# Kernel optimization log

Measured on AMD Instinct MI355X. Metric: run time of the kernel, lower is better.

## Reference

```python
import jax, jax.numpy as jnp
import numpy as np

NBATCH, NA = 16, 1024


def setup_inputs() -> dict:
    key = jax.random.key(0)
    # Batched dense operator parameters; the linear module applies the
    # symmetrized matrix M = 0.5*(A + A^T) (Hermitian operator -> real spectrum).
    A = jax.random.normal(key, (NBATCH, NA, NA), dtype=jnp.float32)
    return {"A": A, "nlowest": 16}


def reference(A, nlowest):
    # EigenModule.forward with method='exacteig': full symmetric
    # eigendecomposition, then keep the `nlowest` lowest eigenpairs.
    M = 0.5 * (A + jnp.swapaxes(A, -1, -2))  # (B, na, na) symmetric
    eigvals, eigvecs = jnp.linalg.eigh(M)    # ascending eigenvalues
    return eigvals[:, :nlowest], eigvecs[:, :, :nlowest]
```

## Files before the change

### kernel.cpp

```cpp
#include <hip/hip_runtime.h>
#include <stdint.h>
#include <math.h>

#define NN 1024
#define NB 16
#define NLOW 16
#define PNB 32
#define JCH 128
#define GMID 4

__device__ inline void patchvals(float alphaf, double rest, float& albe, float& beta, float& taut) {
    if (rest == 0.0) { albe = 0.f; beta = alphaf; taut = 0.f; return; }
    double a = (double)alphaf;
    double nrm = sqrt(a * a + rest);
    double b = (a >= 0.0) ? -nrm : nrm;
    double ab = a - b;
    albe = (float)ab;
    beta = (float)b;
    taut = (float)(-1.0 / (b * ab));
}

__global__ void k_symmetrize(const float* A, float* M) {
    int64_t t = (int64_t)blockIdx.x * blockDim.x + threadIdx.x;
    if (t >= (int64_t)NB * NN * NN) return;
    int b = (int)(t / (NN * NN));
    int rc = (int)(t % (NN * NN));
    int r = rc / NN, c = rc % NN;
    if (r > c) return;
    const float* Ab = A + (int64_t)b * NN * NN;
    float s = 0.5f * (Ab[(int64_t)r * NN + c] + Ab[(int64_t)c * NN + r]);
    float* Mb = M + (int64_t)b * NN * NN;
    Mb[(int64_t)r * NN + c] = s;
    Mb[(int64_t)c * NN + r] = s;
}

__global__ void k_zeroinit(float* wv, double* norm2A, double* dotwA) {
    int t = blockIdx.x * 256 + threadIdx.x;
    if (t < NB * NN) { wv[t] = 0.f; norm2A[t] = 0.0; dotwA[t] = 0.0; }
}

__global__ __launch_bounds__(256) void k_midA(const float* Vp, float* Wp, float* wv,
                                              const float* tauA, double* dotwA,
                                              const double* c1A, const double* c2A,
                                              int k0, int j) {
    int b = blockIdx.x, y = blockIdx.y, tid = threadIdx.x;
    int jp = j - 1, kp = k0 + jp, m0 = NN - 1 - k0;
    __shared__ float g1[PNB], g2[PNB];
    __shared__ double redd[256];
    if (tid < jp) {
        double kap = 0.5 * (double)tauA[b * NN + k0 + tid] * dotwA[b * NN + k0 + tid];
        double c2 = c2A[b * PNB + tid];
        g1[tid] = (float)(c1A[b * PNB + tid] - 2.0 * kap * c2);
        g2[tid] = (float)c2;
    }
    __syncthreads();
    float taut = tauA[b * NN + kp];
    const float* ujp = Vp + ((int64_t)b * PNB + jp) * NN;
    float* wcol = Wp + ((int64_t)b * PNB + jp) * NN;
    double dacc = 0.0;
    for (int i = jp + y * 256 + tid; i < m0; i += GMID * 256) {
        float wr = wv[b * NN + i];
        wv[b * NN + i] = 0.f;
        for (int t = 0; t < jp; ++t)
            wr -= Vp[((int64_t)b * PNB + t) * NN + i] * g1[t]
                + Wp[((int64_t)b * PNB + t) * NN + i] * g2[t];
        float wf = taut * wr;
        wcol[i] = wf;
        dacc += (double)wf * (double)ujp[i];
    }
    redd[tid] = dacc; __syncthreads();
    for (int s = 128; s > 0; s >>= 1) {
        if (tid < s) redd[tid] += redd[tid + s];
        __syncthreads();
    }
    if (tid == 0) atomicAdd(&dotwA[b * NN + kp], redd[0]);
}

__global__ __launch_bounds__(256) void k_midB(float* M, float* Vp, const float* Wp,
                                              float* dA, const float* tauA, const double* dotwA,
                                              double* norm2A, float* alphaA,
                                              int k0, int j) {
    int b = blockIdx.x, y = blockIdx.y, tid = threadIdx.x;
    int k = k0 + j, m0 = NN - 1 - k0;
    float* Mb = M + (int64_t)b * NN * NN;
    __shared__ float h1[PNB], h2[PNB], h3[PNB];
    __shared__ double redd[256];
    if (tid < j) {
        int r = j - 1;
        float ur = Vp[((int64_t)b * PNB + tid) * NN + r];
        float wr = Wp[((int64_t)b * PNB + tid) * NN + r];
        float kap = (float)(0.5 * (double)tauA[b * NN + k0 + tid] * dotwA[b * NN + k0 + tid]);
        float wbar = wr - kap * ur;
        h1[tid] = wbar - kap * ur;
        h2[tid] = ur;
        h3[tid] = ur * wbar;
    }
    __syncthreads();
    if (y == 0 && tid == 0) {
        float dk = Mb[(int64_t)k * NN + k];
        for (int t = 0; t < j; ++t) dk -= 2.f * h3[t];
        dA[b * NN + k] = dk;
    }
    double nacc = 0.0;
    float* ucol = Vp + ((int64_t)b * PNB + j) * NN;
    for (int i = j + y * 256 + tid; i < m0; i += GMID * 256) {
        float x = Mb[(int64_t)(k0 + 1 + i) * NN + k];
        for (int t = 0; t < j; ++t)
            x -= Vp[((int64_t)b * PNB + t) * NN + i] * h1[t]
               + Wp[((int64_t)b * PNB + t) * NN + i] * h2[t];
        ucol[i] = x;
        Mb[(int64_t)(k0 + 1 + i) * NN + k] = x;
        if (i == j) alphaA[b * NN + k] = x;
        else nacc += (double)x * (double)x;
    }
    redd[tid] = nacc; __syncthreads();
    for (int s = 128; s > 0; s >>= 1) {
        if (tid < s) redd[tid] += redd[tid + s];
        __syncthreads();
    }
    if (tid == 0) atomicAdd(&norm2A[b * NN + k], redd[0]);
}

__global__ __launch_bounds__(256) void k_symv(float* M, float* Vp, const float* Wp,
                                              float* wv, float* tauA, float* eA,
                                              const float* alphaA, const double* norm2A,
                                              double* c1A, double* c2A,
                                              int k0, int j, int nr, int nc) {
    int b = blockIdx.x, y = blockIdx.y, tid = threadIdx.x;
    int k = k0 + j, m = NN - 1 - k, base = k + 1, m0 = NN - 1 - k0;
    float albe, beta, taut;
    patchvals(alphaA[b * NN + k], norm2A[b * NN + k], albe, beta, taut);
    float* Mb = M + (int64_t)b * NN * NN;
    float* ucol = Vp + ((int64_t)b * PNB + j) * NN;
    __shared__ float vs[JCH];
    __shared__ double r1[256], r2[256];
    if (y < nr * nc) {
        if (y == 0 && tid == 0) {
            ucol[j] = albe;
            Mb[(int64_t)(k0 + 1 + j) * NN + k] = albe;
            eA[b * NN + k] = beta;
            tauA[b * NN + k] = taut;
        }
        int ir = y % nr, ic = y / nr;
        int i = ir * 256 + tid;
        int jg0 = ic * JCH, jg1 = min(m, jg0 + JCH);
        for (int t = tid; t < jg1 - jg0; t += 256) vs[t] = ucol[jg0 + t + j];
        __syncthreads();
        if (tid == 0 && jg0 == 0) vs[0] = albe;
        __syncthreads();
        if (i < m) {
            const float* p = Mb + (int64_t)(base + jg0) * NN + base + i;
            float acc = 0.f;
            for (int jg = jg0; jg < jg1; ++jg, p += NN) acc += (*p) * vs[jg - jg0];
            atomicAdd(&wv[b * NN + i + j], acc);
        }
    } else {
        int t = y - nr * nc;
        const float* ut = Vp + ((int64_t)b * PNB + t) * NN;
        const float* wt = Wp + ((int64_t)b * PNB + t) * NN;
        double a1 = 0.0, a2 = 0.0;
        for (int i = j + tid; i < m0; i += 256) {
            float uj = (i == j) ? albe : ucol[i];
            a1 += (double)wt[i] * (double)uj;
            a2 += (double)ut[i] * (double)uj;
        }
        r1[tid] = a1; r2[tid] = a2; __syncthreads();
        for (int s = 128; s > 0; s >>= 1) {
            if (tid < s) { r1[tid] += r1[tid + s]; r2[tid] += r2[tid + s]; }
            __syncthreads();
        }
        if (tid == 0) { c1A[b * PNB + t] = r1[0]; c2A[b * PNB + t] = r2[0]; }
    }
}

__global__ __launch_bounds__(256) void k_update(float* M, const float* Vp, const float* Wp,
                                                const float* tauA, const double* dotwA,
                                                int k0, int nbe) {
    int b = blockIdx.x;
    int s = k0 + nbe, m2 = NN - s;
    int r0 = blockIdx.y * 64, c0 = blockIdx.z * 64;
    if (r0 >= m2 || c0 >= m2) return;
    __shared__ float Vr[PNB][64], Wr[PNB][64], Vc[PNB][64], Wc[PNB][64];
    __shared__ float kap[PNB];
    int tid = threadIdx.x;
    if (tid < nbe)
        kap[tid] = (float)(0.5 * (double)tauA[b * NN + k0 + tid] * dotwA[b * NN + k0 + tid]);
    __syncthreads();
    int rowoff = nbe - 1;
    for (int idx = tid; idx < nbe * 64; idx += 256) {
        int t = idx >> 6, x = idx & 63;
        const float* vp = Vp + ((int64_t)b * PNB + t) * NN;
        const float* wp = Wp + ((int64_t)b * PNB + t) * NN;
        int rr = r0 + x, cc = c0 + x;
        float vr = (rr < m2) ? vp[rowoff + rr] : 0.f;
        float wr = (rr < m2) ? wp[rowoff + rr] : 0.f;
        float vc = (cc < m2) ? vp[rowoff + cc] : 0.f;
        float wc = (cc < m2) ? wp[rowoff + cc] : 0.f;
        Vr[t][x] = vr; Wr[t][x] = wr - kap[t] * vr;
        Vc[t][x] = vc; Wc[t][x] = wc - kap[t] * vc;
    }
    __syncthreads();
    int tx = tid & 15, ty = tid >> 4;
    float accv[4][4] = {};
    for (int t = 0; t < nbe; ++t) {
        float va[4], wa[4], vb4[4], wb4[4];
#pragma unroll
        for (int a = 0; a < 4; ++a) {
            va[a] = Vr[t][ty * 4 + a]; wa[a] = Wr[t][ty * 4 + a];
            vb4[a] = Vc[t][tx * 4 + a]; wb4[a] = Wc[t][tx * 4 + a];
        }
#pragma unroll
        for (int a = 0; a < 4; ++a)
#pragma unroll
            for (int c = 0; c < 4; ++c) accv[a][c] += va[a] * wb4[c] + wa[a] * vb4[c];
    }
    float* Mb = M + (int64_t)b * NN * NN;
    for (int a = 0; a < 4; ++a) {
        int r = r0 + ty * 4 + a;
        if (r >= m2) break;
        for (int c = 0; c < 4; ++c) {
            int cc = c0 + tx * 4 + c;
            if (cc >= m2) continue;
            Mb[(int64_t)(s + r) * NN + (s + cc)] -= accv[a][c];
        }
    }
}

__global__ void k_extract2(const float* M, float* dA, float* eA) {
    int b = blockIdx.x;
    if (threadIdx.x == 0) {
        const float* Mb = M + (int64_t)b * NN * NN;
        dA[b * NN + NN - 2] = Mb[(int64_t)(NN - 2) * NN + NN - 2];
        dA[b * NN + NN - 1] = Mb[(int64_t)(NN - 1) * NN + NN - 1];
        eA[b * NN + NN - 2] = Mb[(int64_t)(NN - 1) * NN + NN - 2];
    }
}

__global__ void k_bisect(const float* dA, const float* eA, double* lam, float* out) {
    int p = threadIdx.x;
    int b = p >> 4, j = p & 15;
    const float* d = dA + b * NN;
    const float* e = eA + b * NN;
    double lo = 1e30, hi = -1e30;
    for (int i = 0; i < NN; ++i) {
        double di = (double)d[i];
        double r = 0.0;
        if (i > 0) r += fabs((double)e[i - 1]);
        if (i < NN - 1) r += fabs((double)e[i]);
        lo = fmin(lo, di - r);
        hi = fmax(hi, di + r);
    }
    lo -= 1e-3; hi += 1e-3;
    for (int it = 0; it < 50; ++it) {
        double x = 0.5 * (lo + hi);
        int cnt = 0;
        double q = (double)d[0] - x;
        if (q < 0.0) cnt++;
        for (int i = 1; i < NN; ++i) {
            double ei = (double)e[i - 1];
            double den = q;
            if (fabs(den) < 1e-30) den = (den < 0.0) ? -1e-30 : 1e-30;
            q = ((double)d[i] - x) - ei * ei / den;
            if (q < 0.0) cnt++;
        }
        if (cnt >= j + 1) hi = x; else lo = x;
    }
    double l = 0.5 * (lo + hi);
    lam[p] = l;
    out[b * NLOW + j] = (float)l;
}

__global__ void k_invit(const float* dA, const float* eA, const double* lam,
                        float* vtri, double* U0, double* U1, double* U2,
                        double* LM, float* PV, double* XV) {
    int p = blockIdx.x * blockDim.x + threadIdx.x;
    if (p >= NB * NLOW) return;
    int b = p / NLOW;
    const float* d = dA + b * NN;
    const float* e = eA + b * NN;
    double lambda = lam[p];
    double* dd  = U0 + (int64_t)p * NN;
    double* du  = U1 + (int64_t)p * NN;
    double* du2 = U2 + (int64_t)p * NN;
    double* dl  = LM + (int64_t)p * NN;
    float*  pv  = PV + (int64_t)p * NN;
    double* X   = XV + (int64_t)p * NN;

    for (int i = 0; i < NN; ++i) dd[i] = (double)d[i] - lambda;
    for (int i = 0; i < NN - 1; ++i) { du[i] = (double)e[i]; dl[i] = (double)e[i]; }
    du[NN - 1] = 0.0; dl[NN - 1] = 0.0;

    for (int i = 0; i < NN - 1; ++i) {
        if (fabs(dd[i]) >= fabs(dl[i])) {
            pv[i] = 0.f;
            double fact = (dd[i] != 0.0) ? dl[i] / dd[i] : 0.0;
            dl[i] = fact;
            dd[i + 1] -= fact * du[i];
            du2[i] = 0.0;
        } else {
            pv[i] = 1.f;
            double fact = dd[i] / dl[i];
            dd[i] = dl[i];
            dl[i] = fact;
            double temp = du[i];
            du[i] = dd[i + 1];
            dd[i + 1] = temp - fact * dd[i + 1];
            if (i < NN - 2) { du2[i] = du[i + 1]; du[i + 1] = -fact * du[i + 1]; }
            else du2[i] = 0.0;
        }
    }
    for (int i = 0; i < NN; ++i)
        if (fabs(dd[i]) < 1e-300) dd[i] = (dd[i] < 0.0) ? -1e-300 : 1e-300;

    for (int i = 0; i < NN; ++i) {
        uint32_t h = ((uint32_t)i * 2654435761u) ^ ((uint32_t)p * 40503u);
        h = h * 1664525u + 1013904223u;
        X[i] = 1.0 + 1e-3 * ((double)(h & 2047) / 1024.0 - 1.0);
    }
    for (int iter = 0; iter < 2; ++iter) {
        for (int i = 0; i < NN - 1; ++i) {
            if (pv[i] == 0.f) X[i + 1] -= dl[i] * X[i];
            else { double t = X[i]; X[i] = X[i + 1]; X[i + 1] = t - dl[i] * X[i]; }
        }
        X[NN - 1] /= dd[NN - 1];
        X[NN - 2] = (X[NN - 2] - du[NN - 2] * X[NN - 1]) / dd[NN - 2];
        for (int i = NN - 3; i >= 0; --i)
            X[i] = (X[i] - du[i] * X[i + 1] - du2[i] * X[i + 2]) / dd[i];
        double nrm = 0.0;
        for (int i = 0; i < NN; ++i) nrm += X[i] * X[i];
        double inv = 1.0 / sqrt(fmax(nrm, 1e-300));
        for (int i = 0; i < NN; ++i) X[i] *= inv;
    }
    float* vt = vtri + (int64_t)p * NN;
    for (int i = 0; i < NN; ++i) vt[i] = (float)X[i];
}

__global__ void k_gs(float* vtri) {
    int b = blockIdx.x;
    float* V = vtri + (int64_t)b * NLOW * NN;
    __shared__ double red[256];
    for (int j = 0; j < NLOW; ++j) {
        float* vj = V + j * NN;
        for (int i2 = 0; i2 < j; ++i2) {
            const float* vi = V + i2 * NN;
            double acc = 0.0;
            for (int t = threadIdx.x; t < NN; t += 256) acc += (double)vi[t] * (double)vj[t];
            red[threadIdx.x] = acc; __syncthreads();
            for (int s = 128; s > 0; s >>= 1) {
                if ((int)threadIdx.x < s) red[threadIdx.x] += red[threadIdx.x + s];
                __syncthreads();
            }
            float r = (float)red[0];
            for (int t = threadIdx.x; t < NN; t += 256) vj[t] -= r * vi[t];
            __syncthreads();
        }
        double acc = 0.0;
        for (int t = threadIdx.x; t < NN; t += 256) acc += (double)vj[t] * (double)vj[t];
        red[threadIdx.x] = acc; __syncthreads();
        for (int s = 128; s > 0; s >>= 1) {
            if ((int)threadIdx.x < s) red[threadIdx.x] += red[threadIdx.x + s];
            __syncthreads();
        }
        float inv = (float)(1.0 / sqrt(fmax(red[0], 1e-300)));
        for (int t = threadIdx.x; t < NN; t += 256) vj[t] *= inv;
        __syncthreads();
    }
}

__global__ __launch_bounds__(512) void k_backtransform(const float* M, const float* tauA,
                                                       const float* vtri, float* out) {
    int b = blockIdx.x;
    int pass = blockIdx.y;
    int w = threadIdx.x >> 6;
    int lane = threadIdx.x & 63;
    int j = pass * 8 + w;
    __shared__ float xs[8][NN];
    __shared__ float us[NN];
    const float* Mb = M + (int64_t)b * NN * NN;
    for (int i = lane; i < NN; i += 64)
        xs[w][i] = vtri[((int64_t)b * NLOW + j) * NN + i];
    __syncthreads();
    for (int k = NN - 3; k >= 0; --k) {
        int m = NN - 1 - k;
        for (int t = threadIdx.x; t < (unsigned)m; t += 512)
            us[t] = Mb[(int64_t)(k + 1 + t) * NN + k];
        __syncthreads();
        float tauk = tauA[b * NN + k];
        float acc = 0.f;
        for (int t = lane; t < m; t += 64) acc += us[t] * xs[w][k + 1 + t];
        for (int off = 32; off > 0; off >>= 1) acc += __shfl_xor(acc, off);
        float s = tauk * acc;
        for (int t = lane; t < m; t += 64) xs[w][k + 1 + t] -= s * us[t];
        __syncthreads();
    }
    float mx = -1.f; int mi = 0;
    for (int i = lane; i < NN; i += 64) {
        float a = fabsf(xs[w][i]);
        if (a > mx) { mx = a; mi = i; }
    }
    for (int off = 32; off > 0; off >>= 1) {
        float omx = __shfl_xor(mx, off);
        int omi = __shfl_xor(mi, off);
        if (omx > mx || (omx == mx && omi < mi)) { mx = omx; mi = omi; }
    }
    float sgn = (xs[w][mi] < 0.f) ? -1.f : 1.f;
    for (int i = lane; i < NN; i += 64)
        out[256 + ((int64_t)(b * NN + i)) * NLOW + j] = sgn * xs[w][i];
}

extern "C" void kernel_launch(void* const* d_in, const int* in_sizes, int n_in,
                              void* d_out, int out_size, void* d_ws, size_t ws_size,
                              hipStream_t stream) {
    const float* A = (const float*)d_in[0];
    float* out = (float*)d_out;

    char* base = (char*)d_ws;
    size_t off = 0;
    auto alloc = [&](size_t bytes) -> void* {
        void* p = (void*)(base + off);
        off = (off + bytes + 255) & ~(size_t)255;
        return p;
    };
    double* lam  = (double*)alloc(sizeof(double) * NB * NLOW);
    double* u0   = (double*)alloc(sizeof(double) * (size_t)NB * NLOW * NN);
    double* u1   = (double*)alloc(sizeof(double) * (size_t)NB * NLOW * NN);
    double* u2   = (double*)alloc(sizeof(double) * (size_t)NB * NLOW * NN);
    double* lmul = (double*)alloc(sizeof(double) * (size_t)NB * NLOW * NN);
    double* xv   = (double*)alloc(sizeof(double) * (size_t)NB * NLOW * NN);
    float* pivf  = (float*)alloc(sizeof(float) * (size_t)NB * NLOW * NN);
    float* vtri  = (float*)alloc(sizeof(float) * (size_t)NB * NLOW * NN);
    float* tau   = (float*)alloc(sizeof(float) * NB * NN);
    float* evec  = (float*)alloc(sizeof(float) * NB * NN);
    float* dvec  = (float*)alloc(sizeof(float) * NB * NN);
    float* wv    = (float*)alloc(sizeof(float) * NB * NN);
    float* alphaA = (float*)alloc(sizeof(float) * NB * NN);
    double* norm2A = (double*)alloc(sizeof(double) * NB * NN);
    double* dotwA  = (double*)alloc(sizeof(double) * NB * NN);
    double* c1A    = (double*)alloc(sizeof(double) * NB * PNB);
    double* c2A    = (double*)alloc(sizeof(double) * NB * PNB);
    float* Vp    = (float*)alloc(sizeof(float) * (size_t)NB * PNB * NN);
    float* Wp    = (float*)alloc(sizeof(float) * (size_t)NB * PNB * NN);
    size_t small_end = off;

    float* M;
    if (ws_size >= small_end + sizeof(float) * (size_t)NB * NN * NN)
        M = (float*)alloc(sizeof(float) * (size_t)NB * NN * NN);
    else
        M = (float*)d_in[0];

    int grid_sym = (NB * NN * NN) / 256;
    k_symmetrize<<<grid_sym, 256, 0, stream>>>(A, M);
    k_zeroinit<<<(NB * NN + 255) / 256, 256, 0, stream>>>(wv, norm2A, dotwA);

    for (int k0 = 0; k0 < NN - 2; k0 += PNB) {
        int jmax = NN - 2 - k0; if (jmax > PNB) jmax = PNB;
        for (int j = 0; j < jmax; ++j) {
            if (j > 0)
                k_midA<<<dim3(NB, GMID), 256, 0, stream>>>(Vp, Wp, wv, tau, dotwA, c1A, c2A, k0, j);
            k_midB<<<dim3(NB, GMID), 256, 0, stream>>>(M, Vp, Wp, dvec, tau, dotwA, norm2A, alphaA, k0, j);
            int k = k0 + j, m = NN - 1 - k;
            int nr = (m + 255) / 256, nc = (m + JCH - 1) / JCH;
            k_symv<<<dim3(NB, nr * nc + j), 256, 0, stream>>>(M, Vp, Wp, wv, tau, evec,
                                                              alphaA, norm2A, c1A, c2A,
                                                              k0, j, nr, nc);
        }
        k_midA<<<dim3(NB, GMID), 256, 0, stream>>>(Vp, Wp, wv, tau, dotwA, c1A, c2A, k0, jmax);
        int s = k0 + jmax, m2 = NN - s;
        if (m2 > 0) {
            dim3 gu(NB, (unsigned)((m2 + 63) / 64), (unsigned)((m2 + 63) / 64));
            k_update<<<gu, 256, 0, stream>>>(M, Vp, Wp, tau, dotwA, k0, jmax);
        }
    }

    k_extract2<<<NB, 64, 0, stream>>>(M, dvec, evec);
    k_bisect<<<1, 256, 0, stream>>>(dvec, evec, lam, out);
    k_invit<<<4, 64, 0, stream>>>(dvec, evec, lam, vtri, u0, u1, u2, lmul, pivf, xv);
    k_gs<<<NB, 256, 0, stream>>>(vtri);
    dim3 gI(NB, 2);
    k_backtransform<<<gI, 512, 0, stream>>>(M, tau, vtri, out);
}
```

Measured before the change: 41.04 ms.

## Fuse panel mid-step kernels into one per-batch block and store Householder vectors contiguously

Merges k_midA and k_midB into a single 1024-thread kernel per batch. It computes the Householder reflector in-block, which removes the norm/alpha atomics and the patchvals recomputation, and moves the c1/c2 dot products out of the symv launch into that kernel. k_symv becomes a pure matvec with a larger column chunk. A contiguous copy of each Householder vector (Urev) is also stored when workspace permits, so back-transformation reads rows instead of strided columns. This cuts launch count and per-step synchronization at the cost of fewer, larger blocks in the mid step and an extra matrix-sized workspace buffer.

```diff
diff --git a/kernel.cpp b/kernel.cpp
--- a/kernel.cpp
+++ b/kernel.cpp
@@ -6,19 +6,7 @@
 #define NB 16
 #define NLOW 16
 #define PNB 32
-#define JCH 128
-#define GMID 4
-
-__device__ inline void patchvals(float alphaf, double rest, float& albe, float& beta, float& taut) {
-    if (rest == 0.0) { albe = 0.f; beta = alphaf; taut = 0.f; return; }
-    double a = (double)alphaf;
-    double nrm = sqrt(a * a + rest);
-    double b = (a >= 0.0) ? -nrm : nrm;
-    double ab = a - b;
-    albe = (float)ab;
-    beta = (float)b;
-    taut = (float)(-1.0 / (b * ab));
-}
+#define JCH 256
 
 __global__ void k_symmetrize(const float* A, float* M) {
     int64_t t = (int64_t)blockIdx.x * blockDim.x + threadIdx.x;
@@ -34,57 +22,63 @@
     Mb[(int64_t)c * NN + r] = s;
 }
 
-__global__ void k_zeroinit(float* wv, double* norm2A, double* dotwA) {
+__global__ void k_zeroinit(float* wv) {
     int t = blockIdx.x * 256 + threadIdx.x;
-    if (t < NB * NN) { wv[t] = 0.f; norm2A[t] = 0.0; dotwA[t] = 0.0; }
-}
-
-__global__ __launch_bounds__(256) void k_midA(const float* Vp, float* Wp, float* wv,
-                                              const float* tauA, double* dotwA,
-                                              const double* c1A, const double* c2A,
-                                              int k0, int j) {
-    int b = blockIdx.x, y = blockIdx.y, tid = threadIdx.x;
-    int jp = j - 1, kp = k0 + jp, m0 = NN - 1 - k0;
-    __shared__ float g1[PNB], g2[PNB];
-    __shared__ double redd[256];
-    if (tid < jp) {
-        double kap = 0.5 * (double)tauA[b * NN + k0 + tid] * dotwA[b * NN + k0 + tid];
-        double c2 = c2A[b * PNB + tid];
-        g1[tid] = (float)(c1A[b * PNB + tid] - 2.0 * kap * c2);
-        g2[tid] = (float)c2;
-    }
-    __syncthreads();
-    float taut = tauA[b * NN + kp];
-    const float* ujp = Vp + ((int64_t)b * PNB + jp) * NN;
-    float* wcol = Wp + ((int64_t)b * PNB + jp) * NN;
-    double dacc = 0.0;
-    for (int i = jp + y * 256 + tid; i < m0; i += GMID * 256) {
-        float wr = wv[b * NN + i];
-        wv[b * NN + i] = 0.f;
-        for (int t = 0; t < jp; ++t)
-            wr -= Vp[((int64_t)b * PNB + t) * NN + i] * g1[t]
-                + Wp[((int64_t)b * PNB + t) * NN + i] * g2[t];
-        float wf = taut * wr;
-        wcol[i] = wf;
-        dacc += (double)wf * (double)ujp[i];
-    }
-    redd[tid] = dacc; __syncthreads();
-    for (int s = 128; s > 0; s >>= 1) {
-        if (tid < s) redd[tid] += redd[tid + s];
-        __syncthreads();
-    }
-    if (tid == 0) atomicAdd(&dotwA[b * NN + kp], redd[0]);
-}
-
-__global__ __launch_bounds__(256) void k_midB(float* M, float* Vp, const float* Wp,
-                                              float* dA, const float* tauA, const double* dotwA,
-                                              double* norm2A, float* alphaA,
-                                              int k0, int j) {
-    int b = blockIdx.x, y = blockIdx.y, tid = threadIdx.x;
-    int k = k0 + j, m0 = NN - 1 - k0;
+    if (t < NB * NN) wv[t] = 0.f;
+}
+
+__global__ __launch_bounds__(1024) void k_mid(float* M, float* Vp, float* Wp, float* wv,
+                                              float* tauA, float* eA, float* dA,
+                                              double* dotwA, double* c1A, double* c2A,
+                                              float* Urev, int useU,
+                                              int k0, int j, int do_col) {
+    int b = blockIdx.x, tid = threadIdx.x;
+    int wid = tid >> 6, lane = tid & 63;
+    int m0 = NN - 1 - k0;
     float* Mb = M + (int64_t)b * NN * NN;
-    __shared__ float h1[PNB], h2[PNB], h3[PNB];
-    __shared__ double redd[256];
+    __shared__ double sred[16];
+    __shared__ float g1[PNB], g2[PNB], h1[PNB], h2[PNB], h3[PNB];
+    __shared__ float shu[NN];
+    __shared__ float sc_alpha, sc_albe;
+
+    if (j > 0) {
+        int jp = j - 1, kp = k0 + jp;
+        if (tid < jp) {
+            double kap = 0.5 * (double)tauA[b * NN + k0 + tid] * dotwA[b * NN + k0 + tid];
+            double c2 = c2A[b * PNB + tid];
+            g1[tid] = (float)(c1A[b * PNB + tid] - 2.0 * kap * c2);
+            g2[tid] = (float)c2;
+        }
+        __syncthreads();
+        float taut = tauA[b * NN + kp];
+        const float* ujp = Vp + ((int64_t)b * PNB + jp) * NN;
+        float* wcol = Wp + ((int64_t)b * PNB + jp) * NN;
+        int i = jp + tid;
+        double dacc = 0.0;
+        if (i < m0) {
+            float wr = wv[b * NN + i];
+            wv[b * NN + i] = 0.f;
+            for (int t = 0; t < jp; ++t)
+                wr -= Vp[((int64_t)b * PNB + t) * NN + i] * g1[t]
+                    + Wp[((int64_t)b * PNB + t) * NN + i] * g2[t];
+            float wf = taut * wr;
+            wcol[i] = wf;
+            dacc = (double)wf * (double)ujp[i];
+        }
+        for (int o = 32; o; o >>= 1) dacc += __shfl_xor(dacc, o);
+        if (lane == 0) sred[wid] = dacc;
+        __syncthreads();
+        if (tid == 0) {
+            double tot = 0.0;
+            for (int w = 0; w < 16; ++w) tot += sred[w];
+            dotwA[b * NN + kp] = tot;
+        }
+        __syncthreads();
+    }
+
+    if (!do_col) return;
+
+    int k = k0 + j;
     if (tid < j) {
         int r = j - 1;
         float ur = Vp[((int64_t)b * PNB + tid) * NN + r];
@@ -96,81 +90,80 @@
         h3[tid] = ur * wbar;
     }
     __syncthreads();
-    if (y == 0 && tid == 0) {
+    int i = j + tid;
+    float x = 0.f;
+    if (i < m0) {
+        x = Mb[(int64_t)(k0 + 1 + i) * NN + k];
+        for (int t = 0; t < j; ++t)
+            x -= Vp[((int64_t)b * PNB + t) * NN + i] * h1[t]
+               + Wp[((int64_t)b * PNB + t) * NN + i] * h2[t];
+    }
+    if (tid == 0) sc_alpha = x;
+    double nacc = (i > j && i < m0) ? (double)x * (double)x : 0.0;
+    for (int o = 32; o; o >>= 1) nacc += __shfl_xor(nacc, o);
+    if (lane == 0) sred[wid] = nacc;
+    __syncthreads();
+    if (tid == 0) {
+        double rest = 0.0;
+        for (int w = 0; w < 16; ++w) rest += sred[w];
+        float albe, beta, taut;
+        if (rest == 0.0) { albe = 0.f; beta = sc_alpha; taut = 0.f; }
+        else {
+            double a = (double)sc_alpha;
+            double nrm = sqrt(a * a + rest);
+            double bt = (a >= 0.0) ? -nrm : nrm;
+            double ab = a - bt;
+            albe = (float)ab;
+            beta = (float)bt;
+            taut = (float)(-1.0 / (bt * ab));
+        }
         float dk = Mb[(int64_t)k * NN + k];
         for (int t = 0; t < j; ++t) dk -= 2.f * h3[t];
         dA[b * NN + k] = dk;
-    }
-    double nacc = 0.0;
-    float* ucol = Vp + ((int64_t)b * PNB + j) * NN;
-    for (int i = j + y * 256 + tid; i < m0; i += GMID * 256) {
-        float x = Mb[(int64_t)(k0 + 1 + i) * NN + k];
-        for (int t = 0; t < j; ++t)
-            x -= Vp[((int64_t)b * PNB + t) * NN + i] * h1[t]
-               + Wp[((int64_t)b * PNB + t) * NN + i] * h2[t];
-        ucol[i] = x;
-        Mb[(int64_t)(k0 + 1 + i) * NN + k] = x;
-        if (i == j) alphaA[b * NN + k] = x;
-        else nacc += (double)x * (double)x;
-    }
-    redd[tid] = nacc; __syncthreads();
-    for (int s = 128; s > 0; s >>= 1) {
-        if (tid < s) redd[tid] += redd[tid + s];
-        __syncthreads();
-    }
-    if (tid == 0) atomicAdd(&norm2A[b * NN + k], redd[0]);
-}
-
-__global__ __launch_bounds__(256) void k_symv(float* M, float* Vp, const float* Wp,
-                                              float* wv, float* tauA, float* eA,
-                                              const float* alphaA, const double* norm2A,
-                                              double* c1A, double* c2A,
-                                              int k0, int j, int nr, int nc) {
-    int b = blockIdx.x, y = blockIdx.y, tid = threadIdx.x;
-    int k = k0 + j, m = NN - 1 - k, base = k + 1, m0 = NN - 1 - k0;
-    float albe, beta, taut;
-    patchvals(alphaA[b * NN + k], norm2A[b * NN + k], albe, beta, taut);
-    float* Mb = M + (int64_t)b * NN * NN;
-    float* ucol = Vp + ((int64_t)b * PNB + j) * NN;
-    __shared__ float vs[JCH];
-    __shared__ double r1[256], r2[256];
-    if (y < nr * nc) {
-        if (y == 0 && tid == 0) {
-            ucol[j] = albe;
-            Mb[(int64_t)(k0 + 1 + j) * NN + k] = albe;
-            eA[b * NN + k] = beta;
-            tauA[b * NN + k] = taut;
-        }
-        int ir = y % nr, ic = y / nr;
-        int i = ir * 256 + tid;
-        int jg0 = ic * JCH, jg1 = min(m, jg0 + JCH);
-        for (int t = tid; t < jg1 - jg0; t += 256) vs[t] = ucol[jg0 + t + j];
-        __syncthreads();
-        if (tid == 0 && jg0 == 0) vs[0] = albe;
-        __syncthreads();
-        if (i < m) {
-            const float* p = Mb + (int64_t)(base + jg0) * NN + base + i;
-            float acc = 0.f;
-            for (int jg = jg0; jg < jg1; ++jg, p += NN) acc += (*p) * vs[jg - jg0];
-            atomicAdd(&wv[b * NN + i + j], acc);
-        }
-    } else {
-        int t = y - nr * nc;
+        tauA[b * NN + k] = taut;
+        eA[b * NN + k] = beta;
+        sc_albe = albe;
+    }
+    __syncthreads();
+    if (i < m0) {
+        float val = (tid == 0) ? sc_albe : x;
+        Vp[((int64_t)b * PNB + j) * NN + i] = val;
+        Mb[(int64_t)(k0 + 1 + i) * NN + k] = val;
+        if (useU) Urev[((int64_t)b * NN + k) * NN + (i - j)] = val;
+        shu[i] = val;
+    }
+    __syncthreads();
+    for (int t = wid; t < j; t += 16) {
         const float* ut = Vp + ((int64_t)b * PNB + t) * NN;
         const float* wt = Wp + ((int64_t)b * PNB + t) * NN;
         double a1 = 0.0, a2 = 0.0;
-        for (int i = j + tid; i < m0; i += 256) {
-            float uj = (i == j) ? albe : ucol[i];
-            a1 += (double)wt[i] * (double)uj;
-            a2 += (double)ut[i] * (double)uj;
-        }
-        r1[tid] = a1; r2[tid] = a2; __syncthreads();
-        for (int s = 128; s > 0; s >>= 1) {
-            if (tid < s) { r1[tid] += r1[tid + s]; r2[tid] += r2[tid + s]; }
-            __syncthreads();
-        }
-        if (tid == 0) { c1A[b * PNB + t] = r1[0]; c2A[b * PNB + t] = r2[0]; }
-    }
+        for (int i2 = j + lane; i2 < m0; i2 += 64) {
+            float uj = shu[i2];
+            a1 += (double)wt[i2] * (double)uj;
+            a2 += (double)ut[i2] * (double)uj;
+        }
+        for (int o = 32; o; o >>= 1) { a1 += __shfl_xor(a1, o); a2 += __shfl_xor(a2, o); }
+        if (lane == 0) { c1A[b * PNB + t] = a1; c2A[b * PNB + t] = a2; }
+    }
+}
+
+__global__ __launch_bounds__(256) void k_symv(const float* M, const float* Vp, float* wv,
+                                              int k0, int j) {
+    int b = blockIdx.x;
+    int k = k0 + j, m = NN - 1 - k, base = k + 1;
+    int i = blockIdx.y * 256 + threadIdx.x;
+    int jg0 = blockIdx.z * JCH;
+    int jg1 = min(m, jg0 + JCH);
+    __shared__ float vs[JCH];
+    const float* vcol = Vp + ((int64_t)b * PNB + j) * NN;
+    for (int t = threadIdx.x; t < jg1 - jg0; t += 256) vs[t] = vcol[jg0 + t + j];
+    __syncthreads();
+    if (i >= m) return;
+    const float* Mb = M + (int64_t)b * NN * NN;
+    const float* p = Mb + (int64_t)(base + jg0) * NN + base + i;
+    float acc = 0.f;
+    for (int jg = jg0; jg < jg1; ++jg, p += NN) acc += (*p) * vs[jg - jg0];
+    atomicAdd(&wv[b * NN + i + j], acc);
 }
 
 __global__ __launch_bounds__(256) void k_update(float* M, const float* Vp, const float* Wp,
@@ -367,7 +360,8 @@
     }
 }
 
-__global__ __launch_bounds__(512) void k_backtransform(const float* M, const float* tauA,
+__global__ __launch_bounds__(512) void k_backtransform(const float* M, const float* Urev,
+                                                       int useU, const float* tauA,
                                                        const float* vtri, float* out) {
     int b = blockIdx.x;
     int pass = blockIdx.y;
@@ -382,8 +376,13 @@
     __syncthreads();
     for (int k = NN - 3; k >= 0; --k) {
         int m = NN - 1 - k;
-        for (int t = threadIdx.x; t < (unsigned)m; t += 512)
-            us[t] = Mb[(int64_t)(k + 1 + t) * NN + k];
+        if (useU) {
+            const float* ur = Urev + ((int64_t)b * NN + k) * NN;
+            for (int t = threadIdx.x; t < (unsigned)m; t += 512) us[t] = ur[t];
+        } else {
+            for (int t = threadIdx.x; t < (unsigned)m; t += 512)
+                us[t] = Mb[(int64_t)(k + 1 + t) * NN + k];
+        }
         __syncthreads();
         float tauk = tauA[b * NN + k];
         float acc = 0.f;
@@ -433,38 +432,42 @@
     float* evec  = (float*)alloc(sizeof(float) * NB * NN);
     float* dvec  = (float*)alloc(sizeof(float) * NB * NN);
     float* wv    = (float*)alloc(sizeof(float) * NB * NN);
-    float* alphaA = (float*)alloc(sizeof(float) * NB * NN);
-    double* norm2A = (double*)alloc(sizeof(double) * NB * NN);
-    double* dotwA  = (double*)alloc(sizeof(double) * NB * NN);
-    double* c1A    = (double*)alloc(sizeof(double) * NB * PNB);
-    double* c2A    = (double*)alloc(sizeof(double) * NB * PNB);
+    double* dotwA = (double*)alloc(sizeof(double) * NB * NN);
+    double* c1A   = (double*)alloc(sizeof(double) * NB * PNB);
+    double* c2A   = (double*)alloc(sizeof(double) * NB * PNB);
     float* Vp    = (float*)alloc(sizeof(float) * (size_t)NB * PNB * NN);
     float* Wp    = (float*)alloc(sizeof(float) * (size_t)NB * PNB * NN);
     size_t small_end = off;
+    size_t mat_bytes = sizeof(float) * (size_t)NB * NN * NN;
 
     float* M;
-    if (ws_size >= small_end + sizeof(float) * (size_t)NB * NN * NN)
-        M = (float*)alloc(sizeof(float) * (size_t)NB * NN * NN);
+    if (ws_size >= small_end + mat_bytes)
+        M = (float*)alloc(mat_bytes);
     else
         M = (float*)d_in[0];
 
+    float* Urev = nullptr;
+    int useU = 0;
+    if (ws_size >= off + mat_bytes) {
+        Urev = (float*)alloc(mat_bytes);
+        useU = 1;
+    }
+
     int grid_sym = (NB * NN * NN) / 256;
     k_symmetrize<<<grid_sym, 256, 0, stream>>>(A, M);
-    k_zeroinit<<<(NB * NN + 255) / 256, 256, 0, stream>>>(wv, norm2A, dotwA);
+    k_zeroinit<<<(NB * NN + 255) / 256, 256, 0, stream>>>(wv);
 
     for (int k0 = 0; k0 < NN - 2; k0 += PNB) {
         int jmax = NN - 2 - k0; if (jmax > PNB) jmax = PNB;
         for (int j = 0; j < jmax; ++j) {
-            if (j > 0)
-                k_midA<<<dim3(NB, GMID), 256, 0, stream>>>(Vp, Wp, wv, tau, dotwA, c1A, c2A, k0, j);
-            k_midB<<<dim3(NB, GMID), 256, 0, stream>>>(M, Vp, Wp, dvec, tau, dotwA, norm2A, alphaA, k0, j);
+            k_mid<<<NB, 1024, 0, stream>>>(M, Vp, Wp, wv, tau, evec, dvec,
+                                           dotwA, c1A, c2A, Urev, useU, k0, j, 1);
             int k = k0 + j, m = NN - 1 - k;
             int nr = (m + 255) / 256, nc = (m + JCH - 1) / JCH;
-            k_symv<<<dim3(NB, nr * nc + j), 256, 0, stream>>>(M, Vp, Wp, wv, tau, evec,
-                                                              alphaA, norm2A, c1A, c2A,
-                                                              k0, j, nr, nc);
-        }
-        k_midA<<<dim3(NB, GMID), 256, 0, stream>>>(Vp, Wp, wv, tau, dotwA, c1A, c2A, k0, jmax);
+            k_symv<<<dim3(NB, nr, nc), 256, 0, stream>>>(M, Vp, wv, k0, j);
+        }
+        k_mid<<<NB, 1024, 0, stream>>>(M, Vp, Wp, wv, tau, evec, dvec,
+                                       dotwA, c1A, c2A, Urev, useU, k0, jmax, 0);
         int s = k0 + jmax, m2 = NN - s;
         if (m2 > 0) {
             dim3 gu(NB, (unsigned)((m2 + 63) / 64), (unsigned)((m2 + 63) / 64));
@@ -477,5 +480,5 @@
     k_invit<<<4, 64, 0, stream>>>(dvec, evec, lam, vtri, u0, u1, u2, lmul, pivf, xv);
     k_gs<<<NB, 256, 0, stream>>>(vtri);
     dim3 gI(NB, 2);
-    k_backtransform<<<gI, 512, 0, stream>>>(M, tau, vtri, out);
-}
+    k_backtransform<<<gI, 512, 0, stream>>>(M, Urev, useU, tau, vtri, out);
+}
```

Result: slower. 59.39 ms (+44.7%).

## Fuse panel mid kernels, compute dot products algebraically, store reflectors contiguously

Applied to the files above, without the earlier changes.

Merges the two per-column panel kernels into one launch, cutting the launch count per column roughly in half. The w·u dot product is now derived algebraically from a q = u·(A u) accumulation done inside the symv, replacing a separate reduction and atomic pass. Householder vectors are written to a separate row-contiguous buffer when workspace allows, so the backtransform reads coalesced rows instead of strided columns. The symv column chunk doubles, and bisection is spread across four blocks. The algebraic dot product can lose precision through cancellation, and the new buffer costs a second full matrix of workspace.

```diff
diff --git a/kernel.cpp b/kernel.cpp
--- a/kernel.cpp
+++ b/kernel.cpp
@@ -6,7 +6,7 @@
 #define NB 16
 #define NLOW 16
 #define PNB 32
-#define JCH 128
+#define JCH 256
 #define GMID 4
 
 __device__ inline void patchvals(float alphaf, double rest, float& albe, float& beta, float& taut) {
@@ -34,102 +34,115 @@
     Mb[(int64_t)c * NN + r] = s;
 }
 
-__global__ void k_zeroinit(float* wv, double* norm2A, double* dotwA) {
+__global__ void k_zeroinit(float* wv, double* norm2A, double* qA, double* dotwA) {
     int t = blockIdx.x * 256 + threadIdx.x;
-    if (t < NB * NN) { wv[t] = 0.f; norm2A[t] = 0.0; dotwA[t] = 0.0; }
-}
-
-__global__ __launch_bounds__(256) void k_midA(const float* Vp, float* Wp, float* wv,
-                                              const float* tauA, double* dotwA,
-                                              const double* c1A, const double* c2A,
-                                              int k0, int j) {
-    int b = blockIdx.x, y = blockIdx.y, tid = threadIdx.x;
-    int jp = j - 1, kp = k0 + jp, m0 = NN - 1 - k0;
-    __shared__ float g1[PNB], g2[PNB];
-    __shared__ double redd[256];
-    if (tid < jp) {
-        double kap = 0.5 * (double)tauA[b * NN + k0 + tid] * dotwA[b * NN + k0 + tid];
-        double c2 = c2A[b * PNB + tid];
-        g1[tid] = (float)(c1A[b * PNB + tid] - 2.0 * kap * c2);
-        g2[tid] = (float)c2;
-    }
-    __syncthreads();
-    float taut = tauA[b * NN + kp];
-    const float* ujp = Vp + ((int64_t)b * PNB + jp) * NN;
-    float* wcol = Wp + ((int64_t)b * PNB + jp) * NN;
-    double dacc = 0.0;
-    for (int i = jp + y * 256 + tid; i < m0; i += GMID * 256) {
-        float wr = wv[b * NN + i];
-        wv[b * NN + i] = 0.f;
-        for (int t = 0; t < jp; ++t)
-            wr -= Vp[((int64_t)b * PNB + t) * NN + i] * g1[t]
-                + Wp[((int64_t)b * PNB + t) * NN + i] * g2[t];
-        float wf = taut * wr;
-        wcol[i] = wf;
-        dacc += (double)wf * (double)ujp[i];
-    }
-    redd[tid] = dacc; __syncthreads();
-    for (int s = 128; s > 0; s >>= 1) {
-        if (tid < s) redd[tid] += redd[tid + s];
-        __syncthreads();
-    }
-    if (tid == 0) atomicAdd(&dotwA[b * NN + kp], redd[0]);
-}
-
-__global__ __launch_bounds__(256) void k_midB(float* M, float* Vp, const float* Wp,
-                                              float* dA, const float* tauA, const double* dotwA,
-                                              double* norm2A, float* alphaA,
-                                              int k0, int j) {
-    int b = blockIdx.x, y = blockIdx.y, tid = threadIdx.x;
-    int k = k0 + j, m0 = NN - 1 - k0;
+    if (t < NB * NN) { wv[t] = 0.f; norm2A[t] = 0.0; qA[t] = 0.0; dotwA[t] = 0.0; }
+}
+
+__global__ __launch_bounds__(256) void k_midAB(
+    float* M, float* Vp, float* Wp, float* wv,
+    float* tauA, float* dA, double* dotwA, const double* qA,
+    const double* c1A, const double* c2A,
+    double* norm2A, float* alphaA, float* Urev, int useU,
+    int k0, int j, int do_col)
+{
+    int b = blockIdx.x, g = blockIdx.y, tid = threadIdx.x;
+    int m0 = NN - 1 - k0;
+    int k = k0 + j, jp = j - 1;
     float* Mb = M + (int64_t)b * NN * NN;
+    float* VpB = Vp + (int64_t)b * PNB * NN;
+    float* WpB = Wp + (int64_t)b * PNB * NN;
+    __shared__ float skap[PNB], sg1[PNB], sg2[PNB];
+    __shared__ double sc1d[PNB], sc2d[PNB];
     __shared__ float h1[PNB], h2[PNB], h3[PNB];
-    __shared__ double redd[256];
-    if (tid < j) {
-        int r = j - 1;
-        float ur = Vp[((int64_t)b * PNB + tid) * NN + r];
-        float wr = Wp[((int64_t)b * PNB + tid) * NN + r];
-        float kap = (float)(0.5 * (double)tauA[b * NN + k0 + tid] * dotwA[b * NN + k0 + tid]);
-        float wbar = wr - kap * ur;
-        h1[tid] = wbar - kap * ur;
+
+    int base = (j > 0) ? jp : 0;
+    int i = base + g * 256 + tid;
+    double dotw = 0.0;
+    float taut = 0.f;
+
+    if (j > 0) {
+        if (tid < jp) {
+            double kap = 0.5 * (double)tauA[b * NN + k0 + tid] * dotwA[b * NN + k0 + tid];
+            double c1v = c1A[b * PNB + tid], c2v = c2A[b * PNB + tid];
+            skap[tid] = (float)kap;
+            sg1[tid] = (float)(c1v - 2.0 * kap * c2v);
+            sg2[tid] = (float)c2v;
+            sc1d[tid] = c1v; sc2d[tid] = c2v;
+        }
+        __syncthreads();
+        taut = tauA[b * NN + k0 + jp];
+        {
+            double s = 0.0;
+            for (int t = 0; t < jp; ++t)
+                s += 2.0 * sc1d[t] * sc2d[t] - 2.0 * (double)skap[t] * sc2d[t] * sc2d[t];
+            dotw = (double)taut * (qA[b * NN + k0 + jp] - s);
+        }
+        if (i < m0) {
+            float wr = wv[b * NN + i];
+            if (i != jp) wv[b * NN + i] = 0.f;
+            for (int t = 0; t < jp; ++t)
+                wr -= VpB[t * NN + i] * sg1[t] + WpB[t * NN + i] * sg2[t];
+            WpB[jp * NN + i] = taut * wr;
+        }
+        if (g == 0 && tid == 0) dotwA[b * NN + k0 + jp] = dotw;
+    }
+
+    if (!do_col) {
+        __syncthreads();
+        for (int z = g * 256 + tid; z <= jp; z += GMID * 256) wv[b * NN + z] = 0.f;
+        return;
+    }
+
+    if (j > 0 && tid <= jp) {
+        int r = jp;
+        float ur = VpB[tid * NN + r];
+        float wpr, kapt;
+        if (tid < jp) { wpr = WpB[tid * NN + r]; kapt = skap[tid]; }
+        else {
+            float wr = wv[b * NN + jp];
+            for (int t = 0; t < jp; ++t)
+                wr -= VpB[t * NN + r] * sg1[t] + WpB[t * NN + r] * sg2[t];
+            wpr = taut * wr;
+            kapt = (float)(0.5 * (double)taut * dotw);
+        }
+        float wbar = wpr - kapt * ur;
+        h1[tid] = wbar - kapt * ur;
         h2[tid] = ur;
         h3[tid] = ur * wbar;
     }
     __syncthreads();
-    if (y == 0 && tid == 0) {
+
+    float x = 0.f;
+    if (i >= j && i < m0) {
+        x = Mb[(int64_t)(k0 + 1 + i) * NN + k];
+        for (int t = 0; t < j; ++t)
+            x -= VpB[t * NN + i] * h1[t] + WpB[t * NN + i] * h2[t];
+        VpB[j * NN + i] = x;
+        if (useU) Urev[((int64_t)b * NN + k) * NN + (i - j)] = x;
+        else      Mb[(int64_t)(k0 + 1 + i) * NN + k] = x;
+        if (i == j) alphaA[b] = x;
+    }
+    if (g == 0 && tid == 0) {
         float dk = Mb[(int64_t)k * NN + k];
         for (int t = 0; t < j; ++t) dk -= 2.f * h3[t];
         dA[b * NN + k] = dk;
     }
-    double nacc = 0.0;
-    float* ucol = Vp + ((int64_t)b * PNB + j) * NN;
-    for (int i = j + y * 256 + tid; i < m0; i += GMID * 256) {
-        float x = Mb[(int64_t)(k0 + 1 + i) * NN + k];
-        for (int t = 0; t < j; ++t)
-            x -= Vp[((int64_t)b * PNB + t) * NN + i] * h1[t]
-               + Wp[((int64_t)b * PNB + t) * NN + i] * h2[t];
-        ucol[i] = x;
-        Mb[(int64_t)(k0 + 1 + i) * NN + k] = x;
-        if (i == j) alphaA[b * NN + k] = x;
-        else nacc += (double)x * (double)x;
-    }
-    redd[tid] = nacc; __syncthreads();
-    for (int s = 128; s > 0; s >>= 1) {
-        if (tid < s) redd[tid] += redd[tid + s];
-        __syncthreads();
-    }
-    if (tid == 0) atomicAdd(&norm2A[b * NN + k], redd[0]);
+    double nacc = (i > j && i < m0) ? (double)x * (double)x : 0.0;
+    for (int o = 32; o; o >>= 1) nacc += __shfl_xor(nacc, o);
+    if ((tid & 63) == 0) atomicAdd(&norm2A[b * NN + k], nacc);
 }
 
 __global__ __launch_bounds__(256) void k_symv(float* M, float* Vp, const float* Wp,
                                               float* wv, float* tauA, float* eA,
                                               const float* alphaA, const double* norm2A,
-                                              double* c1A, double* c2A,
+                                              double* qA, double* c1A, double* c2A,
+                                              float* Urev, int useU,
                                               int k0, int j, int nr, int nc) {
     int b = blockIdx.x, y = blockIdx.y, tid = threadIdx.x;
     int k = k0 + j, m = NN - 1 - k, base = k + 1, m0 = NN - 1 - k0;
     float albe, beta, taut;
-    patchvals(alphaA[b * NN + k], norm2A[b * NN + k], albe, beta, taut);
+    patchvals(alphaA[b], norm2A[b * NN + k], albe, beta, taut);
     float* Mb = M + (int64_t)b * NN * NN;
     float* ucol = Vp + ((int64_t)b * PNB + j) * NN;
     __shared__ float vs[JCH];
@@ -137,7 +150,8 @@
     if (y < nr * nc) {
         if (y == 0 && tid == 0) {
             ucol[j] = albe;
-            Mb[(int64_t)(k0 + 1 + j) * NN + k] = albe;
+            if (useU) Urev[((int64_t)b * NN + k) * NN] = albe;
+            else      Mb[(int64_t)(k0 + 1 + j) * NN + k] = albe;
             eA[b * NN + k] = beta;
             tauA[b * NN + k] = taut;
         }
@@ -148,21 +162,26 @@
         __syncthreads();
         if (tid == 0 && jg0 == 0) vs[0] = albe;
         __syncthreads();
+        double qp = 0.0;
         if (i < m) {
             const float* p = Mb + (int64_t)(base + jg0) * NN + base + i;
             float acc = 0.f;
             for (int jg = jg0; jg < jg1; ++jg, p += NN) acc += (*p) * vs[jg - jg0];
             atomicAdd(&wv[b * NN + i + j], acc);
-        }
+            float urow = (i == 0) ? albe : ucol[j + i];
+            qp = (double)acc * (double)urow;
+        }
+        for (int o = 32; o; o >>= 1) qp += __shfl_xor(qp, o);
+        if ((tid & 63) == 0) atomicAdd(&qA[b * NN + k], qp);
     } else {
         int t = y - nr * nc;
         const float* ut = Vp + ((int64_t)b * PNB + t) * NN;
         const float* wt = Wp + ((int64_t)b * PNB + t) * NN;
         double a1 = 0.0, a2 = 0.0;
-        for (int i = j + tid; i < m0; i += 256) {
-            float uj = (i == j) ? albe : ucol[i];
-            a1 += (double)wt[i] * (double)uj;
-            a2 += (double)ut[i] * (double)uj;
+        for (int i2 = j + tid; i2 < m0; i2 += 256) {
+            float uj = (i2 == j) ? albe : ucol[i2];
+            a1 += (double)wt[i2] * (double)uj;
+            a2 += (double)ut[i2] * (double)uj;
         }
         r1[tid] = a1; r2[tid] = a2; __syncthreads();
         for (int s = 128; s > 0; s >>= 1) {
@@ -237,7 +256,8 @@
 }
 
 __global__ void k_bisect(const float* dA, const float* eA, double* lam, float* out) {
-    int p = threadIdx.x;
+    int p = blockIdx.x * 64 + threadIdx.x;
+    if (p >= NB * NLOW) return;
     int b = p >> 4, j = p & 15;
     const float* d = dA + b * NN;
     const float* e = eA + b * NN;
@@ -253,17 +273,17 @@
     lo -= 1e-3; hi += 1e-3;
     for (int it = 0; it < 50; ++it) {
         double x = 0.5 * (lo + hi);
-        int cnt = 0;
+        int cntn = 0;
         double q = (double)d[0] - x;
-        if (q < 0.0) cnt++;
+        if (q < 0.0) cntn++;
         for (int i = 1; i < NN; ++i) {
             double ei = (double)e[i - 1];
             double den = q;
             if (fabs(den) < 1e-30) den = (den < 0.0) ? -1e-30 : 1e-30;
             q = ((double)d[i] - x) - ei * ei / den;
-            if (q < 0.0) cnt++;
-        }
-        if (cnt >= j + 1) hi = x; else lo = x;
+            if (q < 0.0) cntn++;
+        }
+        if (cntn >= j + 1) hi = x; else lo = x;
     }
     double l = 0.5 * (lo + hi);
     lam[p] = l;
@@ -367,7 +387,8 @@
     }
 }
 
-__global__ __launch_bounds__(512) void k_backtransform(const float* M, const float* tauA,
+__global__ __launch_bounds__(512) void k_backtransform(const float* M, const float* Urev,
+                                                       int useU, const float* tauA,
                                                        const float* vtri, float* out) {
     int b = blockIdx.x;
     int pass = blockIdx.y;
@@ -382,8 +403,13 @@
     __syncthreads();
     for (int k = NN - 3; k >= 0; --k) {
         int m = NN - 1 - k;
-        for (int t = threadIdx.x; t < (unsigned)m; t += 512)
-            us[t] = Mb[(int64_t)(k + 1 + t) * NN + k];
+        if (useU) {
+            const float* ur = Urev + ((int64_t)b * NN + k) * NN;
+            for (int t = threadIdx.x; t < (unsigned)m; t += 512) us[t] = ur[t];
+        } else {
+            for (int t = threadIdx.x; t < (unsigned)m; t += 512)
+                us[t] = Mb[(int64_t)(k + 1 + t) * NN + k];
+        }
         __syncthreads();
         float tauk = tauA[b * NN + k];
         float acc = 0.f;
@@ -433,38 +459,49 @@
     float* evec  = (float*)alloc(sizeof(float) * NB * NN);
     float* dvec  = (float*)alloc(sizeof(float) * NB * NN);
     float* wv    = (float*)alloc(sizeof(float) * NB * NN);
-    float* alphaA = (float*)alloc(sizeof(float) * NB * NN);
+    float* alphaA = (float*)alloc(sizeof(float) * NB);
     double* norm2A = (double*)alloc(sizeof(double) * NB * NN);
+    double* qA     = (double*)alloc(sizeof(double) * NB * NN);
     double* dotwA  = (double*)alloc(sizeof(double) * NB * NN);
     double* c1A    = (double*)alloc(sizeof(double) * NB * PNB);
     double* c2A    = (double*)alloc(sizeof(double) * NB * PNB);
     float* Vp    = (float*)alloc(sizeof(float) * (size_t)NB * PNB * NN);
     float* Wp    = (float*)alloc(sizeof(float) * (size_t)NB * PNB * NN);
     size_t small_end = off;
+    size_t mat_bytes = sizeof(float) * (size_t)NB * NN * NN;
 
     float* M;
-    if (ws_size >= small_end + sizeof(float) * (size_t)NB * NN * NN)
-        M = (float*)alloc(sizeof(float) * (size_t)NB * NN * NN);
+    if (ws_size >= small_end + mat_bytes)
+        M = (float*)alloc(mat_bytes);
     else
         M = (float*)d_in[0];
 
+    float* Urev = nullptr;
+    int useU = 0;
+    if (ws_size >= off + mat_bytes) {
+        Urev = (float*)alloc(mat_bytes);
+        useU = 1;
+    }
+
     int grid_sym = (NB * NN * NN) / 256;
     k_symmetrize<<<grid_sym, 256, 0, stream>>>(A, M);
-    k_zeroinit<<<(NB * NN + 255) / 256, 256, 0, stream>>>(wv, norm2A, dotwA);
+    k_zeroinit<<<(NB * NN + 255) / 256, 256, 0, stream>>>(wv, norm2A, qA, dotwA);
 
     for (int k0 = 0; k0 < NN - 2; k0 += PNB) {
         int jmax = NN - 2 - k0; if (jmax > PNB) jmax = PNB;
         for (int j = 0; j < jmax; ++j) {
-            if (j > 0)
-                k_midA<<<dim3(NB, GMID), 256, 0, stream>>>(Vp, Wp, wv, tau, dotwA, c1A, c2A, k0, j);
-            k_midB<<<dim3(NB, GMID), 256, 0, stream>>>(M, Vp, Wp, dvec, tau, dotwA, norm2A, alphaA, k0, j);
+            k_midAB<<<dim3(NB, GMID), 256, 0, stream>>>(M, Vp, Wp, wv, tau, dvec,
+                                                        dotwA, qA, c1A, c2A, norm2A,
+                                                        alphaA, Urev, useU, k0, j, 1);
             int k = k0 + j, m = NN - 1 - k;
             int nr = (m + 255) / 256, nc = (m + JCH - 1) / JCH;
             k_symv<<<dim3(NB, nr * nc + j), 256, 0, stream>>>(M, Vp, Wp, wv, tau, evec,
-                                                              alphaA, norm2A, c1A, c2A,
-                                                              k0, j, nr, nc);
-        }
-        k_midA<<<dim3(NB, GMID), 256, 0, stream>>>(Vp, Wp, wv, tau, dotwA, c1A, c2A, k0, jmax);
+                                                              alphaA, norm2A, qA, c1A, c2A,
+                                                              Urev, useU, k0, j, nr, nc);
+        }
+        k_midAB<<<dim3(NB, GMID), 256, 0, stream>>>(M, Vp, Wp, wv, tau, dvec,
+                                                    dotwA, qA, c1A, c2A, norm2A,
+                                                    alphaA, Urev, useU, k0, jmax, 0);
         int s = k0 + jmax, m2 = NN - s;
         if (m2 > 0) {
             dim3 gu(NB, (unsigned)((m2 + 63) / 64), (unsigned)((m2 + 63) / 64));
@@ -473,9 +510,9 @@
     }
 
     k_extract2<<<NB, 64, 0, stream>>>(M, dvec, evec);
-    k_bisect<<<1, 256, 0, stream>>>(dvec, evec, lam, out);
+    k_bisect<<<4, 64, 0, stream>>>(dvec, evec, lam, out);
     k_invit<<<4, 64, 0, stream>>>(dvec, evec, lam, vtri, u0, u1, u2, lmul, pivf, xv);
     k_gs<<<NB, 256, 0, stream>>>(vtri);
     dim3 gI(NB, 2);
-    k_backtransform<<<gI, 512, 0, stream>>>(M, tau, vtri, out);
-}
+    k_backtransform<<<gI, 512, 0, stream>>>(M, Urev, useU, tau, vtri, out);
+}
```

Result: slower. 59.21 ms (+44.3%).
